# Kernel tuning notes

Measured on AMD Instinct MI355X. Metric: run time of the kernel, lower is better.

## Reference

```python
import jax, jax.numpy as jnp
import numpy as np

N, D, K_FRAC = 4096, 256, 0.5
EPS = 1e-5  # BatchNorm1d default eps


def setup_inputs() -> dict:
    key = jax.random.key(0)
    kg, kh, kw = jax.random.split(key, 3)
    # sparse binary adjacency with self-loops so all degrees > 0 (pow(D,-1) finite)
    g = (jax.random.uniform(kg, (N, N)) < 0.004).astype(jnp.float32)
    g = jnp.maximum(g, jnp.eye(N, dtype=jnp.float32))
    h = jax.random.normal(kh, (N, D), dtype=jnp.float32)
    return {
        "g": g,
        "h": h,
        "gamma": jnp.ones((D,), jnp.float32),
        "beta": jnp.zeros((D,), jnp.float32),
        "w_proj": jax.random.normal(kw, (D, 1), dtype=jnp.float32) / np.sqrt(D),
        "b_proj": jnp.zeros((1,), jnp.float32),
        "sigma1": jnp.array([0.2], jnp.float32),
    }


def reference(g, h, gamma, beta, w_proj, b_proj, sigma1):
    # BatchNorm1d in training mode: batch statistics over the node axis
    mu = h.mean(0)
    var = h.var(0)  # biased variance, as torch uses for normalization
    h = (h - mu) / jnp.sqrt(var + EPS) * gamma + beta

    deg = g.sum(1)                               # [N] == Z2
    agg = (g @ h) / deg[:, None]                 # diag(D^-1) @ (g @ h), no NxN diag materialized
    Z1 = jnp.abs(h - agg).sum(1)                 # [N]
    pl = jax.nn.sigmoid(Z1 + deg)
    Z3 = (agg @ w_proj + b_proj)[:, 0]           # proj(Z3).squeeze()
    pg = jax.nn.softmax(Z3)                      # 1-D softmax (dim 0)
    pt = jax.nn.sigmoid(pl + pg)
    pf = jax.nn.sigmoid((h @ w_proj + b_proj)[:, 0])
    scores = sigma1[0] * pt + (1.0 - sigma1[0]) * pf

    # top_k_graph
    k = max(2, int(K_FRAC * N))
    _, idx = jax.lax.top_k(scores, k)            # [k]
    h_att = scores[:, None] * h                  # score-weighted features
    un_g = (g != 0).astype(jnp.float32)
    two_hop = ((un_g @ un_g) != 0).astype(jnp.float32)  # binarized 2-hop adjacency
    a_hat = two_hop[idx, :]                      # [k, N] row gather
    new_h = a_hat @ h_att                        # [k, D]
    g_new = a_hat[:, idx]                        # [k, k] column gather
    # norm_g: torch broadcast divides COLUMN j by row-sum degrees[j]
    g_new = g_new / g_new.sum(1)
    return g_new, new_h, idx
```

## Files before the change

### kernel.cpp

```cpp
#include <hip/hip_runtime.h>
#include <math.h>

#define NN 4096
#define DD 256
#define KK 2048
#define NW 64

__device__ __forceinline__ int build_list(const unsigned long long* __restrict__ B, int r,
                                          int l, int* cols, int cap) {
    unsigned long long word = B[(size_t)r * NW + l];
    int pc = __popcll(word);
    int off = pc;
    for (int d = 1; d < 64; d <<= 1) {
        int n = __shfl_up(off, d);
        if (l >= d) off += n;
    }
    int total = __shfl(off, 63);
    int base = off - pc;
    while (word) {
        int b = (int)__ffsll(word) - 1;
        word &= word - 1;
        if (base < cap) cols[base] = l * 64 + b;
        ++base;
    }
    return total;
}

__global__ void k_pre(const float* __restrict__ h, const float* __restrict__ g,
                      double* __restrict__ psum, double* __restrict__ psq,
                      unsigned long long* __restrict__ B) {
    int blk = blockIdx.x;
    int t = threadIdx.x;
    if (blk < 64) {
        int d = t;
        int r0 = blk * 64;
        double s0=0,s1=0,s2=0,s3=0,q0=0,q1=0,q2=0,q3=0;
        for (int k = 0; k < 64; k += 4) {
            double x0 = (double)h[(size_t)(r0+k+0) * DD + d];
            double x1 = (double)h[(size_t)(r0+k+1) * DD + d];
            double x2 = (double)h[(size_t)(r0+k+2) * DD + d];
            double x3 = (double)h[(size_t)(r0+k+3) * DD + d];
            s0 += x0; q0 += x0*x0;
            s1 += x1; q1 += x1*x1;
            s2 += x2; q2 += x2*x2;
            s3 += x3; q3 += x3*x3;
        }
        psum[blk * DD + d] = (s0+s1)+(s2+s3);
        psq [blk * DD + d] = (q0+q1)+(q2+q3);
    } else {
        int i = blk - 64;
        int q = t >> 6, l = t & 63;
        const float4* g4 = (const float4*)(g + (size_t)i * NN);
        for (int wi = 0; wi < 4; ++wi) {
            float4 v = g4[q * 256 + wi * 64 + l];
            unsigned int nib = (unsigned int)(v.x != 0.f)
                             | ((unsigned int)(v.y != 0.f) << 1)
                             | ((unsigned int)(v.z != 0.f) << 2)
                             | ((unsigned int)(v.w != 0.f) << 3);
            unsigned long long word = (unsigned long long)nib << (4 * (l & 15));
            unsigned int lo = (unsigned int)word, hi = (unsigned int)(word >> 32);
            for (int s = 1; s < 16; s <<= 1) {
                lo |= __shfl_xor(lo, s, 16);
                hi |= __shfl_xor(hi, s, 16);
            }
            if ((l & 15) == 0)
                B[(size_t)i * NW + 16 * q + 4 * wi + (l >> 4)] =
                    ((unsigned long long)hi << 32) | lo;
        }
    }
}

__global__ void k_stats_final(const double* __restrict__ psum, const double* __restrict__ psq,
                              double* __restrict__ mu, double* __restrict__ rstd) {
    __shared__ double rs[4][DD];
    __shared__ double rq[4][DD];
    int t = threadIdx.x;
    int d = t & (DD - 1);
    int q = t >> 8;
    double s0=0,s1=0,q0=0,q1=0;
    int b0 = q * 16;
    for (int k = 0; k < 16; k += 2) {
        s0 += psum[(b0+k)   * DD + d];
        s1 += psum[(b0+k+1) * DD + d];
        q0 += psq [(b0+k)   * DD + d];
        q1 += psq [(b0+k+1) * DD + d];
    }
    rs[q][d] = s0 + s1;
    rq[q][d] = q0 + q1;
    __syncthreads();
    if (q == 0) {
        double S  = (rs[0][d]+rs[1][d]) + (rs[2][d]+rs[3][d]);
        double Q  = (rq[0][d]+rq[1][d]) + (rq[2][d]+rq[3][d]);
        double m  = S / (double)NN;
        double var = Q / (double)NN - m * m;
        mu[d]   = m;
        rstd[d] = 1.0 / sqrt(var + 1e-5);
    }
}

__global__ void k_main(const float* __restrict__ h, const double* __restrict__ mu,
                       const double* __restrict__ rstd, const float* __restrict__ gamma,
                       const float* __restrict__ beta, const unsigned long long* __restrict__ Bm,
                       const float* __restrict__ w, const float* __restrict__ bp,
                       float* __restrict__ hn, double* __restrict__ zpf,
                       unsigned long long* __restrict__ T, double* __restrict__ Z1,
                       double* __restrict__ Z3, int* __restrict__ degi) {
    __shared__ int cols[4][136];
    int blk = blockIdx.x;
    int t = threadIdx.x;
    int wv = t >> 6, l = t & 63;
    if (blk < 1024) {
        int r = blk * 4 + wv;
        int cnt = build_list(Bm, r, l, cols[wv], 128);
        if (cnt > 128) cnt = 128;
        const float4* h4 = (const float4*)h;
        double s0=0,s1=0,s2=0,s3=0,u0=0,u1=0,u2=0,u3=0;
        int j = 0;
        for (; j + 1 < cnt; j += 2) {
            float4 v0 = h4[(size_t)cols[wv][j]     * 64 + l];
            float4 v1 = h4[(size_t)cols[wv][j + 1] * 64 + l];
            s0 += (double)v0.x; s1 += (double)v0.y; s2 += (double)v0.z; s3 += (double)v0.w;
            u0 += (double)v1.x; u1 += (double)v1.y; u2 += (double)v1.z; u3 += (double)v1.w;
        }
        if (j < cnt) {
            float4 v0 = h4[(size_t)cols[wv][j] * 64 + l];
            s0 += (double)v0.x; s1 += (double)v0.y; s2 += (double)v0.z; s3 += (double)v0.w;
        }
        s0 += u0; s1 += u1; s2 += u2; s3 += u3;
        const double2* mu2 = (const double2*)mu;
        const double2* rs2 = (const double2*)rstd;
        const float4*  ga4 = (const float4*)gamma;
        const float4*  be4 = (const float4*)beta;
        const float4*  w4  = (const float4*)w;
        double2 mA = mu2[2*l], mB = mu2[2*l+1];
        double2 rA = rs2[2*l], rB = rs2[2*l+1];
        float4 ga = ga4[l], be = be4[l], wl = w4[l];
        double inv = 1.0 / (double)cnt;
        double g0 = (s0 * inv - mA.x) * rA.x * (double)ga.x + (double)be.x;
        double g1 = (s1 * inv - mA.y) * rA.y * (double)ga.y + (double)be.y;
        double g2 = (s2 * inv - mB.x) * rB.x * (double)ga.z + (double)be.z;
        double g3 = (s3 * inv - mB.y) * rB.y * (double)ga.w + (double)be.w;
        float4 hv = h4[(size_t)r * 64 + l];
        double h0 = ((double)hv.x - mA.x) * rA.x * (double)ga.x + (double)be.x;
        double h1 = ((double)hv.y - mA.y) * rA.y * (double)ga.y + (double)be.y;
        double h2 = ((double)hv.z - mB.x) * rB.x * (double)ga.z + (double)be.z;
        double h3 = ((double)hv.w - mB.y) * rB.y * (double)ga.w + (double)be.w;
        float4 o = { (float)h0, (float)h1, (float)h2, (float)h3 };
        ((float4*)hn)[(size_t)r * 64 + l] = o;
        double z1p = (fabs(h0 - g0) + fabs(h1 - g1)) + (fabs(h2 - g2) + fabs(h3 - g3));
        double z3p = (g0 * (double)wl.x + g1 * (double)wl.y)
                   + (g2 * (double)wl.z + g3 * (double)wl.w);
        double zfp = (h0 * (double)wl.x + h1 * (double)wl.y)
                   + (h2 * (double)wl.z + h3 * (double)wl.w);
        for (int off = 32; off > 0; off >>= 1) {
            z1p += __shfl_down(z1p, off);
            z3p += __shfl_down(z3p, off);
            zfp += __shfl_down(zfp, off);
        }
        if (l == 0) {
            Z1[r] = z1p;
            Z3[r] = z3p + (double)bp[0];
            zpf[r] = zfp + (double)bp[0];
            degi[r] = cnt;
        }
    } else {
        int r = (blk - 1024) * 4 + wv;
        int cnt = build_list(Bm, r, l, cols[wv], 128);
        if (cnt > 128) cnt = 128;
        unsigned long long a0 = 0ull, a1 = 0ull;
        int j = 0;
        for (; j + 1 < cnt; j += 2) {
            a0 |= Bm[(size_t)cols[wv][j]     * NW + l];
            a1 |= Bm[(size_t)cols[wv][j + 1] * NW + l];
        }
        if (j < cnt) a0 |= Bm[(size_t)cols[wv][j] * NW + l];
        T[(size_t)r * NW + l] = a0 | a1;
    }
}

__global__ void k_scorekeys(const double* __restrict__ Z1, const double* __restrict__ Z3,
                            const double* __restrict__ zpf, const int* __restrict__ degi,
                            const float* __restrict__ sigma1, float* __restrict__ scores,
                            unsigned long long* __restrict__ keys) {
    __shared__ double red[256];
    int t = threadIdx.x;
    double mx = -1e300;
    for (int k = 0; k < 16; ++k) mx = fmax(mx, Z3[t + 256 * k]);
    red[t] = mx;
    __syncthreads();
    for (int s = 128; s > 0; s >>= 1) {
        if (t < s) red[t] = fmax(red[t], red[t + s]);
        __syncthreads();
    }
    double M = red[0];
    __syncthreads();
    double se = 0.0;
    for (int k = 0; k < 16; ++k) se += exp(Z3[t + 256 * k] - M);
    red[t] = se;
    __syncthreads();
    for (int s = 128; s > 0; s >>= 1) {
        if (t < s) red[t] += red[t + s];
        __syncthreads();
    }
    double sum = red[0];
    int i = blockIdx.x * 256 + t;
    double s1 = (double)sigma1[0];
    double pg = exp(Z3[i] - M) / sum;
    double pl = 1.0 / (1.0 + exp(-(Z1[i] + (double)degi[i])));
    double pt = 1.0 / (1.0 + exp(-(pl + pg)));
    double pf = 1.0 / (1.0 + exp(-zpf[i]));
    float sc = (float)(s1 * pt + (1.0 - s1) * pf);
    scores[i] = sc;
    unsigned int b2 = __float_as_uint(sc);
    unsigned int ka = (b2 & 0x80000000u) ? ~b2 : (b2 ^ 0x80000000u);
    keys[i] = ((unsigned long long)(~ka) << 32) | (unsigned int)i;
}

__global__ void k_rank(const unsigned long long* __restrict__ keys, int* __restrict__ idx_int,
                       float* __restrict__ out_idx) {
    __shared__ unsigned long long Kl[NN];
    int t = threadIdx.x;
    for (int i = t; i < NN; i += 256) Kl[i] = keys[i];
    __syncthreads();
    int il = t >> 4, sub = t & 15;
    int i = blockIdx.x * 16 + il;
    unsigned long long ki = Kl[i];
    int c0 = 0, c1 = 0, c2 = 0, c3 = 0;
    for (int jj = 0; jj < 256; jj += 4) {
        int j = sub + (jj << 4);
        c0 += (Kl[j]      < ki) ? 1 : 0;
        c1 += (Kl[j + 16] < ki) ? 1 : 0;
        c2 += (Kl[j + 32] < ki) ? 1 : 0;
        c3 += (Kl[j + 48] < ki) ? 1 : 0;
    }
    int cnt = (c0 + c1) + (c2 + c3);
    for (int off = 8; off > 0; off >>= 1) cnt += __shfl_down(cnt, off, 16);
    if (sub == 0 && cnt < KK) {
        idx_int[cnt] = i;
        out_idx[cnt] = (float)i;
    }
}

__global__ void k_rowsum(const unsigned long long* __restrict__ T, const int* __restrict__ idx_int,
                         float* __restrict__ inv_rs) {
    __shared__ unsigned long long Sl[NW];
    int t = threadIdx.x;
    Sl[t] = 0ull;
    for (int j = t; j < KK; j += 64) {
        int ii = idx_int[j];
        atomicOr(&Sl[ii >> 6], 1ull << (ii & 63));
    }
    int j = blockIdx.x * 64 + t;
    int r = idx_int[j];
    const unsigned long long* Tr = T + (size_t)r * NW;
    int c0 = 0, c1 = 0, c2 = 0, c3 = 0;
    for (int w = 0; w < NW; w += 4) {
        c0 += __popcll(Tr[w]     & Sl[w]);
        c1 += __popcll(Tr[w + 1] & Sl[w + 1]);
        c2 += __popcll(Tr[w + 2] & Sl[w + 2]);
        c3 += __popcll(Tr[w + 3] & Sl[w + 3]);
    }
    inv_rs[j] = 1.0f / (float)((c0 + c1) + (c2 + c3));
}

__global__ void k_out(const unsigned long long* __restrict__ T, const int* __restrict__ idx_int,
                      const float* __restrict__ inv_rs, const float* __restrict__ scores,
                      const float* __restrict__ hn, float* __restrict__ out_gnew,
                      float* __restrict__ out_newh) {
    __shared__ unsigned long long Tl[NW];
    __shared__ int cols[2048];
    __shared__ int s_cnt;
    __shared__ float4 red[4][64];
    int blk = blockIdx.x;
    int t = threadIdx.x;
    if (blk < KK) {
        int r = blk;
        if (t < NW) Tl[t] = T[(size_t)idx_int[r] * NW + t];
        __syncthreads();
        const int4*   idx4 = (const int4*)idx_int;
        const float4* irs4 = (const float4*)inv_rs;
        float4* out4 = (float4*)(out_gnew + (size_t)r * KK);
        for (int c4 = t; c4 < KK / 4; c4 += 256) {
            int4 jc = idx4[c4];
            float4 iv = irs4[c4];
            float4 o;
            o.x = ((Tl[jc.x >> 6] >> (jc.x & 63)) & 1ull) ? iv.x : 0.0f;
            o.y = ((Tl[jc.y >> 6] >> (jc.y & 63)) & 1ull) ? iv.y : 0.0f;
            o.z = ((Tl[jc.z >> 6] >> (jc.z & 63)) & 1ull) ? iv.z : 0.0f;
            o.w = ((Tl[jc.w >> 6] >> (jc.w & 63)) & 1ull) ? iv.w : 0.0f;
            out4[c4] = o;
        }
    } else {
        int r = blk - KK;
        int wv = t >> 6, l = t & 63;
        if (t < 64) {
            int total = build_list(T, idx_int[r], t, cols, 2048);
            if (t == 63) s_cnt = total;
        }
        __syncthreads();
        int cnt = s_cnt < 2048 ? s_cnt : 2048;
        const float4* hn4 = (const float4*)hn;
        float4 a0 = {0,0,0,0}, a1 = {0,0,0,0}, a2 = {0,0,0,0}, a3 = {0,0,0,0};
        int j = wv;
        for (; j + 12 < cnt; j += 16) {
            int c0 = cols[j], c1 = cols[j + 4], c2 = cols[j + 8], c3 = cols[j + 12];
            float s0 = scores[c0], s1 = scores[c1], s2 = scores[c2], s3 = scores[c3];
            float4 v0 = hn4[(size_t)c0 * 64 + l];
            float4 v1 = hn4[(size_t)c1 * 64 + l];
            float4 v2 = hn4[(size_t)c2 * 64 + l];
            float4 v3 = hn4[(size_t)c3 * 64 + l];
            a0.x = fmaf(s0, v0.x, a0.x); a0.y = fmaf(s0, v0.y, a0.y);
            a0.z = fmaf(s0, v0.z, a0.z); a0.w = fmaf(s0, v0.w, a0.w);
            a1.x = fmaf(s1, v1.x, a1.x); a1.y = fmaf(s1, v1.y, a1.y);
            a1.z = fmaf(s1, v1.z, a1.z); a1.w = fmaf(s1, v1.w, a1.w);
            a2.x = fmaf(s2, v2.x, a2.x); a2.y = fmaf(s2, v2.y, a2.y);
            a2.z = fmaf(s2, v2.z, a2.z); a2.w = fmaf(s2, v2.w, a2.w);
            a3.x = fmaf(s3, v3.x, a3.x); a3.y = fmaf(s3, v3.y, a3.y);
            a3.z = fmaf(s3, v3.z, a3.z); a3.w = fmaf(s3, v3.w, a3.w);
        }
        for (; j < cnt; j += 4) {
            int c0 = cols[j];
            float s0 = scores[c0];
            float4 v0 = hn4[(size_t)c0 * 64 + l];
            a0.x = fmaf(s0, v0.x, a0.x); a0.y = fmaf(s0, v0.y, a0.y);
            a0.z = fmaf(s0, v0.z, a0.z); a0.w = fmaf(s0, v0.w, a0.w);
        }
        float4 acc;
        acc.x = (a0.x + a1.x) + (a2.x + a3.x);
        acc.y = (a0.y + a1.y) + (a2.y + a3.y);
        acc.z = (a0.z + a1.z) + (a2.z + a3.z);
        acc.w = (a0.w + a1.w) + (a2.w + a3.w);
        red[wv][l] = acc;
        __syncthreads();
        if (t < 64) {
            float4 r0 = red[0][t], r1 = red[1][t], r2 = red[2][t], r3 = red[3][t];
            float4 o;
            o.x = (r0.x + r1.x) + (r2.x + r3.x);
            o.y = (r0.y + r1.y) + (r2.y + r3.y);
            o.z = (r0.z + r1.z) + (r2.z + r3.z);
            o.w = (r0.w + r1.w) + (r2.w + r3.w);
            ((float4*)(out_newh + (size_t)r * DD))[t] = o;
        }
    }
}

extern "C" void kernel_launch(void* const* d_in, const int* in_sizes, int n_in,
                              void* d_out, int out_size, void* d_ws, size_t ws_size,
                              hipStream_t stream) {
    const float* g      = (const float*)d_in[0];
    const float* h      = (const float*)d_in[1];
    const float* gamma  = (const float*)d_in[2];
    const float* beta   = (const float*)d_in[3];
    const float* w_proj = (const float*)d_in[4];
    const float* b_proj = (const float*)d_in[5];
    const float* sigma1 = (const float*)d_in[6];

    char* p = (char*)d_ws;
    auto alloc = [&](size_t bytes) -> void* {
        void* q = (void*)p;
        p += (bytes + 255) & ~(size_t)255;
        return q;
    };
    double* mu      = (double*)alloc(DD * 8);
    double* rstd    = (double*)alloc(DD * 8);
    double* psum    = (double*)alloc(64 * DD * 8);
    double* psq     = (double*)alloc(64 * DD * 8);
    double* zpf     = (double*)alloc(NN * 8);
    double* Z1      = (double*)alloc(NN * 8);
    double* Z3      = (double*)alloc(NN * 8);
    int*    degi    = (int*)alloc(NN * 4);
    float*  scores  = (float*)alloc(NN * 4);
    unsigned long long* keys = (unsigned long long*)alloc(NN * 8);
    int*    idx_int = (int*)alloc(KK * 4);
    float*  inv_rs  = (float*)alloc(KK * 4);
    unsigned long long* B = (unsigned long long*)alloc((size_t)NN * NW * 8);
    unsigned long long* T = (unsigned long long*)alloc((size_t)NN * NW * 8);
    float*  hn      = (float*)alloc((size_t)NN * DD * 4);

    float* out_gnew = (float*)d_out;
    float* out_newh = out_gnew + (size_t)KK * KK;
    float* out_idx  = out_newh + (size_t)KK * DD;

    hipLaunchKernelGGL(k_pre,         dim3(64 + NN), dim3(256),  0, stream, h, g, psum, psq, B);
    hipLaunchKernelGGL(k_stats_final, dim3(1),       dim3(1024), 0, stream, psum, psq, mu, rstd);
    hipLaunchKernelGGL(k_main,        dim3(2048),    dim3(256),  0, stream, h, mu, rstd, gamma, beta, B, w_proj, b_proj, hn, zpf, T, Z1, Z3, degi);
    hipLaunchKernelGGL(k_scorekeys,   dim3(16),      dim3(256),  0, stream, Z1, Z3, zpf, degi, sigma1, scores, keys);
    hipLaunchKernelGGL(k_rank,        dim3(256),     dim3(256),  0, stream, keys, idx_int, out_idx);
    hipLaunchKernelGGL(k_rowsum,      dim3(32),      dim3(64),   0, stream, T, idx_int, inv_rs);
    hipLaunchKernelGGL(k_out,         dim3(2 * KK),  dim3(256),  0, stream, T, idx_int, inv_rs, scores, hn, out_gnew, out_newh);
}
```

Measured before the change: 179.8 us.

## Use ballot bitpacking, fuse two-hop OR into aggregation, precompute score-weighted features

The adjacency bitmask is now built with a wave ballot per 64 floats instead of nibble packing plus shuffle reductions. The two-hop OR pass is folded into the main aggregation loop, so the neighbour list is built once per row and the block count is halved. The row-sum kernel is widened to one wave per row with a shuffle reduction. It is merged with a new pass that writes score-scaled features, so the output gather only does adds. The trade-off is an extra N×D buffer written and read, plus more register pressure in the fused main loop.

```diff
diff --git a/kernel.cpp b/kernel.cpp
--- a/kernel.cpp
+++ b/kernel.cpp
@@ -50,23 +50,16 @@
     } else {
         int i = blk - 64;
         int q = t >> 6, l = t & 63;
-        const float4* g4 = (const float4*)(g + (size_t)i * NN);
-        for (int wi = 0; wi < 4; ++wi) {
-            float4 v = g4[q * 256 + wi * 64 + l];
-            unsigned int nib = (unsigned int)(v.x != 0.f)
-                             | ((unsigned int)(v.y != 0.f) << 1)
-                             | ((unsigned int)(v.z != 0.f) << 2)
-                             | ((unsigned int)(v.w != 0.f) << 3);
-            unsigned long long word = (unsigned long long)nib << (4 * (l & 15));
-            unsigned int lo = (unsigned int)word, hi = (unsigned int)(word >> 32);
-            for (int s = 1; s < 16; s <<= 1) {
-                lo |= __shfl_xor(lo, s, 16);
-                hi |= __shfl_xor(hi, s, 16);
-            }
-            if ((l & 15) == 0)
-                B[(size_t)i * NW + 16 * q + 4 * wi + (l >> 4)] =
-                    ((unsigned long long)hi << 32) | lo;
-        }
+        const float* gr = g + (size_t)i * NN;
+        unsigned long long word = 0ull;
+        int lw = l & 15;
+        #pragma unroll
+        for (int wi = 0; wi < 16; ++wi) {
+            float v = gr[(q * 16 + wi) * 64 + l];
+            unsigned long long m = __ballot(v != 0.0f);
+            if (wi == lw) word = m;
+        }
+        if (l < 16) B[(size_t)i * NW + q * 16 + l] = word;
     }
 }
 
@@ -109,72 +102,65 @@
     int blk = blockIdx.x;
     int t = threadIdx.x;
     int wv = t >> 6, l = t & 63;
-    if (blk < 1024) {
-        int r = blk * 4 + wv;
-        int cnt = build_list(Bm, r, l, cols[wv], 128);
-        if (cnt > 128) cnt = 128;
-        const float4* h4 = (const float4*)h;
-        double s0=0,s1=0,s2=0,s3=0,u0=0,u1=0,u2=0,u3=0;
-        int j = 0;
-        for (; j + 1 < cnt; j += 2) {
-            float4 v0 = h4[(size_t)cols[wv][j]     * 64 + l];
-            float4 v1 = h4[(size_t)cols[wv][j + 1] * 64 + l];
-            s0 += (double)v0.x; s1 += (double)v0.y; s2 += (double)v0.z; s3 += (double)v0.w;
-            u0 += (double)v1.x; u1 += (double)v1.y; u2 += (double)v1.z; u3 += (double)v1.w;
-        }
-        if (j < cnt) {
-            float4 v0 = h4[(size_t)cols[wv][j] * 64 + l];
-            s0 += (double)v0.x; s1 += (double)v0.y; s2 += (double)v0.z; s3 += (double)v0.w;
-        }
-        s0 += u0; s1 += u1; s2 += u2; s3 += u3;
-        const double2* mu2 = (const double2*)mu;
-        const double2* rs2 = (const double2*)rstd;
-        const float4*  ga4 = (const float4*)gamma;
-        const float4*  be4 = (const float4*)beta;
-        const float4*  w4  = (const float4*)w;
-        double2 mA = mu2[2*l], mB = mu2[2*l+1];
-        double2 rA = rs2[2*l], rB = rs2[2*l+1];
-        float4 ga = ga4[l], be = be4[l], wl = w4[l];
-        double inv = 1.0 / (double)cnt;
-        double g0 = (s0 * inv - mA.x) * rA.x * (double)ga.x + (double)be.x;
-        double g1 = (s1 * inv - mA.y) * rA.y * (double)ga.y + (double)be.y;
-        double g2 = (s2 * inv - mB.x) * rB.x * (double)ga.z + (double)be.z;
-        double g3 = (s3 * inv - mB.y) * rB.y * (double)ga.w + (double)be.w;
-        float4 hv = h4[(size_t)r * 64 + l];
-        double h0 = ((double)hv.x - mA.x) * rA.x * (double)ga.x + (double)be.x;
-        double h1 = ((double)hv.y - mA.y) * rA.y * (double)ga.y + (double)be.y;
-        double h2 = ((double)hv.z - mB.x) * rB.x * (double)ga.z + (double)be.z;
-        double h3 = ((double)hv.w - mB.y) * rB.y * (double)ga.w + (double)be.w;
-        float4 o = { (float)h0, (float)h1, (float)h2, (float)h3 };
-        ((float4*)hn)[(size_t)r * 64 + l] = o;
-        double z1p = (fabs(h0 - g0) + fabs(h1 - g1)) + (fabs(h2 - g2) + fabs(h3 - g3));
-        double z3p = (g0 * (double)wl.x + g1 * (double)wl.y)
-                   + (g2 * (double)wl.z + g3 * (double)wl.w);
-        double zfp = (h0 * (double)wl.x + h1 * (double)wl.y)
-                   + (h2 * (double)wl.z + h3 * (double)wl.w);
-        for (int off = 32; off > 0; off >>= 1) {
-            z1p += __shfl_down(z1p, off);
-            z3p += __shfl_down(z3p, off);
-            zfp += __shfl_down(zfp, off);
-        }
-        if (l == 0) {
-            Z1[r] = z1p;
-            Z3[r] = z3p + (double)bp[0];
-            zpf[r] = zfp + (double)bp[0];
-            degi[r] = cnt;
-        }
-    } else {
-        int r = (blk - 1024) * 4 + wv;
-        int cnt = build_list(Bm, r, l, cols[wv], 128);
-        if (cnt > 128) cnt = 128;
-        unsigned long long a0 = 0ull, a1 = 0ull;
-        int j = 0;
-        for (; j + 1 < cnt; j += 2) {
-            a0 |= Bm[(size_t)cols[wv][j]     * NW + l];
-            a1 |= Bm[(size_t)cols[wv][j + 1] * NW + l];
-        }
-        if (j < cnt) a0 |= Bm[(size_t)cols[wv][j] * NW + l];
-        T[(size_t)r * NW + l] = a0 | a1;
+    int r = blk * 4 + wv;
+    int cnt = build_list(Bm, r, l, cols[wv], 128);
+    if (cnt > 128) cnt = 128;
+    const float4* h4 = (const float4*)h;
+    double s0=0,s1=0,s2=0,s3=0,u0=0,u1=0,u2=0,u3=0;
+    unsigned long long a0 = 0ull, a1 = 0ull;
+    int j = 0;
+    for (; j + 1 < cnt; j += 2) {
+        int c0 = cols[wv][j], c1 = cols[wv][j + 1];
+        float4 v0 = h4[(size_t)c0 * 64 + l];
+        float4 v1 = h4[(size_t)c1 * 64 + l];
+        a0 |= Bm[(size_t)c0 * NW + l];
+        a1 |= Bm[(size_t)c1 * NW + l];
+        s0 += (double)v0.x; s1 += (double)v0.y; s2 += (double)v0.z; s3 += (double)v0.w;
+        u0 += (double)v1.x; u1 += (double)v1.y; u2 += (double)v1.z; u3 += (double)v1.w;
+    }
+    if (j < cnt) {
+        int c0 = cols[wv][j];
+        float4 v0 = h4[(size_t)c0 * 64 + l];
+        a0 |= Bm[(size_t)c0 * NW + l];
+        s0 += (double)v0.x; s1 += (double)v0.y; s2 += (double)v0.z; s3 += (double)v0.w;
+    }
+    T[(size_t)r * NW + l] = a0 | a1;
+    s0 += u0; s1 += u1; s2 += u2; s3 += u3;
+    const double2* mu2 = (const double2*)mu;
+    const double2* rs2 = (const double2*)rstd;
+    const float4*  ga4 = (const float4*)gamma;
+    const float4*  be4 = (const float4*)beta;
+    const float4*  w4  = (const float4*)w;
+    double2 mA = mu2[2*l], mB = mu2[2*l+1];
+    double2 rA = rs2[2*l], rB = rs2[2*l+1];
+    float4 ga = ga4[l], be = be4[l], wl = w4[l];
+    double inv = 1.0 / (double)cnt;
+    double g0 = (s0 * inv - mA.x) * rA.x * (double)ga.x + (double)be.x;
+    double g1 = (s1 * inv - mA.y) * rA.y * (double)ga.y + (double)be.y;
+    double g2 = (s2 * inv - mB.x) * rB.x * (double)ga.z + (double)be.z;
+    double g3 = (s3 * inv - mB.y) * rB.y * (double)ga.w + (double)be.w;
+    float4 hv = h4[(size_t)r * 64 + l];
+    double h0 = ((double)hv.x - mA.x) * rA.x * (double)ga.x + (double)be.x;
+    double h1 = ((double)hv.y - mA.y) * rA.y * (double)ga.y + (double)be.y;
+    double h2 = ((double)hv.z - mB.x) * rB.x * (double)ga.z + (double)be.z;
+    double h3 = ((double)hv.w - mB.y) * rB.y * (double)ga.w + (double)be.w;
+    float4 o = { (float)h0, (float)h1, (float)h2, (float)h3 };
+    ((float4*)hn)[(size_t)r * 64 + l] = o;
+    double z1p = (fabs(h0 - g0) + fabs(h1 - g1)) + (fabs(h2 - g2) + fabs(h3 - g3));
+    double z3p = (g0 * (double)wl.x + g1 * (double)wl.y)
+               + (g2 * (double)wl.z + g3 * (double)wl.w);
+    double zfp = (h0 * (double)wl.x + h1 * (double)wl.y)
+               + (h2 * (double)wl.z + h3 * (double)wl.w);
+    for (int off = 32; off > 0; off >>= 1) {
+        z1p += __shfl_down(z1p, off);
+        z3p += __shfl_down(z3p, off);
+        zfp += __shfl_down(zfp, off);
+    }
+    if (l == 0) {
+        Z1[r] = z1p;
+        Z3[r] = z3p + (double)bp[0];
+        zpf[r] = zfp + (double)bp[0];
+        degi[r] = cnt;
     }
 }
 
@@ -241,32 +227,42 @@
     }
 }
 
-__global__ void k_rowsum(const unsigned long long* __restrict__ T, const int* __restrict__ idx_int,
-                         float* __restrict__ inv_rs) {
-    __shared__ unsigned long long Sl[NW];
-    int t = threadIdx.x;
-    Sl[t] = 0ull;
-    for (int j = t; j < KK; j += 64) {
-        int ii = idx_int[j];
-        atomicOr(&Sl[ii >> 6], 1ull << (ii & 63));
-    }
-    int j = blockIdx.x * 64 + t;
-    int r = idx_int[j];
-    const unsigned long long* Tr = T + (size_t)r * NW;
-    int c0 = 0, c1 = 0, c2 = 0, c3 = 0;
-    for (int w = 0; w < NW; w += 4) {
-        c0 += __popcll(Tr[w]     & Sl[w]);
-        c1 += __popcll(Tr[w + 1] & Sl[w + 1]);
-        c2 += __popcll(Tr[w + 2] & Sl[w + 2]);
-        c3 += __popcll(Tr[w + 3] & Sl[w + 3]);
-    }
-    inv_rs[j] = 1.0f / (float)((c0 + c1) + (c2 + c3));
+__global__ void k_mid(const unsigned long long* __restrict__ T, const int* __restrict__ idx_int,
+                      const float* __restrict__ scores, const float* __restrict__ hn,
+                      float* __restrict__ inv_rs, float* __restrict__ h_att) {
+    int blk = blockIdx.x;
+    int t = threadIdx.x;
+    if (blk < 128) {
+        __shared__ unsigned long long Sl[NW];
+        if (t < NW) Sl[t] = 0ull;
+        __syncthreads();
+        for (int j = t; j < KK; j += 256) {
+            int ii = idx_int[j];
+            atomicOr(&Sl[ii >> 6], 1ull << (ii & 63));
+        }
+        __syncthreads();
+        int wv = t >> 6, l = t & 63;
+        unsigned long long sw = Sl[l];
+        #pragma unroll
+        for (int k = 0; k < 4; ++k) {
+            int j = blk * 16 + wv * 4 + k;
+            int r = idx_int[j];
+            int c = (int)__popcll(T[(size_t)r * NW + l] & sw);
+            for (int off = 32; off > 0; off >>= 1) c += __shfl_down(c, off);
+            if (l == 0) inv_rs[j] = 1.0f / (float)c;
+        }
+    } else {
+        int i = (blk - 128) * 256 + t;
+        float sc = scores[i >> 6];
+        float4 v = ((const float4*)hn)[i];
+        float4 o = { sc * v.x, sc * v.y, sc * v.z, sc * v.w };
+        ((float4*)h_att)[i] = o;
+    }
 }
 
 __global__ void k_out(const unsigned long long* __restrict__ T, const int* __restrict__ idx_int,
-                      const float* __restrict__ inv_rs, const float* __restrict__ scores,
-                      const float* __restrict__ hn, float* __restrict__ out_gnew,
-                      float* __restrict__ out_newh) {
+                      const float* __restrict__ inv_rs, const float* __restrict__ ha,
+                      float* __restrict__ out_gnew, float* __restrict__ out_newh) {
     __shared__ unsigned long long Tl[NW];
     __shared__ int cols[2048];
     __shared__ int s_cnt;
@@ -299,31 +295,24 @@
         }
         __syncthreads();
         int cnt = s_cnt < 2048 ? s_cnt : 2048;
-        const float4* hn4 = (const float4*)hn;
+        const float4* ha4 = (const float4*)ha;
         float4 a0 = {0,0,0,0}, a1 = {0,0,0,0}, a2 = {0,0,0,0}, a3 = {0,0,0,0};
         int j = wv;
         for (; j + 12 < cnt; j += 16) {
             int c0 = cols[j], c1 = cols[j + 4], c2 = cols[j + 8], c3 = cols[j + 12];
-            float s0 = scores[c0], s1 = scores[c1], s2 = scores[c2], s3 = scores[c3];
-            float4 v0 = hn4[(size_t)c0 * 64 + l];
-            float4 v1 = hn4[(size_t)c1 * 64 + l];
-            float4 v2 = hn4[(size_t)c2 * 64 + l];
-            float4 v3 = hn4[(size_t)c3 * 64 + l];
-            a0.x = fmaf(s0, v0.x, a0.x); a0.y = fmaf(s0, v0.y, a0.y);
-            a0.z = fmaf(s0, v0.z, a0.z); a0.w = fmaf(s0, v0.w, a0.w);
-            a1.x = fmaf(s1, v1.x, a1.x); a1.y = fmaf(s1, v1.y, a1.y);
-            a1.z = fmaf(s1, v1.z, a1.z); a1.w = fmaf(s1, v1.w, a1.w);
-            a2.x = fmaf(s2, v2.x, a2.x); a2.y = fmaf(s2, v2.y, a2.y);
-            a2.z = fmaf(s2, v2.z, a2.z); a2.w = fmaf(s2, v2.w, a2.w);
-            a3.x = fmaf(s3, v3.x, a3.x); a3.y = fmaf(s3, v3.y, a3.y);
-            a3.z = fmaf(s3, v3.z, a3.z); a3.w = fmaf(s3, v3.w, a3.w);
+            float4 v0 = ha4[(size_t)c0 * 64 + l];
+            float4 v1 = ha4[(size_t)c1 * 64 + l];
+            float4 v2 = ha4[(size_t)c2 * 64 + l];
+            float4 v3 = ha4[(size_t)c3 * 64 + l];
+            a0.x += v0.x; a0.y += v0.y; a0.z += v0.z; a0.w += v0.w;
+            a1.x += v1.x; a1.y += v1.y; a1.z += v1.z; a1.w += v1.w;
+            a2.x += v2.x; a2.y += v2.y; a2.z += v2.z; a2.w += v2.w;
+            a3.x += v3.x; a3.y += v3.y; a3.z += v3.z; a3.w += v3.w;
         }
         for (; j < cnt; j += 4) {
             int c0 = cols[j];
-            float s0 = scores[c0];
-            float4 v0 = hn4[(size_t)c0 * 64 + l];
-            a0.x = fmaf(s0, v0.x, a0.x); a0.y = fmaf(s0, v0.y, a0.y);
-            a0.z = fmaf(s0, v0.z, a0.z); a0.w = fmaf(s0, v0.w, a0.w);
+            float4 v0 = ha4[(size_t)c0 * 64 + l];
+            a0.x += v0.x; a0.y += v0.y; a0.z += v0.z; a0.w += v0.w;
         }
         float4 acc;
         acc.x = (a0.x + a1.x) + (a2.x + a3.x);
@@ -376,6 +365,7 @@
     unsigned long long* B = (unsigned long long*)alloc((size_t)NN * NW * 8);
     unsigned long long* T = (unsigned long long*)alloc((size_t)NN * NW * 8);
     float*  hn      = (float*)alloc((size_t)NN * DD * 4);
+    float*  h_att   = (float*)alloc((size_t)NN * DD * 4);
 
     float* out_gnew = (float*)d_out;
     float* out_newh = out_gnew + (size_t)KK * KK;
@@ -383,9 +373,9 @@
 
     hipLaunchKernelGGL(k_pre,         dim3(64 + NN), dim3(256),  0, stream, h, g, psum, psq, B);
     hipLaunchKernelGGL(k_stats_final, dim3(1),       dim3(1024), 0, stream, psum, psq, mu, rstd);
-    hipLaunchKernelGGL(k_main,        dim3(2048),    dim3(256),  0, stream, h, mu, rstd, gamma, beta, B, w_proj, b_proj, hn, zpf, T, Z1, Z3, degi);
+    hipLaunchKernelGGL(k_main,        dim3(1024),    dim3(256),  0, stream, h, mu, rstd, gamma, beta, B, w_proj, b_proj, hn, zpf, T, Z1, Z3, degi);
     hipLaunchKernelGGL(k_scorekeys,   dim3(16),      dim3(256),  0, stream, Z1, Z3, zpf, degi, sigma1, scores, keys);
     hipLaunchKernelGGL(k_rank,        dim3(256),     dim3(256),  0, stream, keys, idx_int, out_idx);
-    hipLaunchKernelGGL(k_rowsum,      dim3(32),      dim3(64),   0, stream, T, idx_int, inv_rs);
-    hipLaunchKernelGGL(k_out,         dim3(2 * KK),  dim3(256),  0, stream, T, idx_int, inv_rs, scores, hn, out_gnew, out_newh);
-}
+    hipLaunchKernelGGL(k_mid,         dim3(128 + 1024), dim3(256), 0, stream, T, idx_int, scores, hn, inv_rs, h_att);
+    hipLaunchKernelGGL(k_out,         dim3(2 * KK),  dim3(256),  0, stream, T, idx_int, inv_rs, h_att, out_gnew, out_newh);
+}
```

Result: faster. 171.9 us (-4.4%).
